# Optimization experiments

Hardware: AMD Instinct MI355X
Metric: run time of the kernel (lower is better)

## Reference

```python
import jax, jax.numpy as jnp
import numpy as np

NUM_ELEC = 128
TIME_STEPS = 128  # must equal NUM_ELEC for the original module's matmuls to be shape-consistent
NUM_VOXELS = 2052
HIDDEN = 64
DCT_DIM = 512
BATCH = 64
RHO = 0.5
TAU = 0.1
PLV_THRESH = 0.5


def dct_matrix(N, K):
    n = np.arange(N)[None, :]
    k = np.arange(K)[:, None]
    m = np.sqrt(2.0 / N) * np.cos(np.pi * (2 * n + 1) * k / (2 * N))
    m[0, :] = 1.0 / np.sqrt(N)
    return jnp.asarray(m, dtype=jnp.float32)


def setup_inputs() -> dict:
    ks = jax.random.split(jax.random.key(0), 12)
    H = HIDDEN
    return {
        "z": jax.random.normal(ks[0], (BATCH, NUM_ELEC, TIME_STEPS), dtype=jnp.float32),
        "lead_field": jax.random.normal(ks[1], (NUM_VOXELS, NUM_ELEC), dtype=jnp.float32),
        "gumbel_u": jax.random.uniform(ks[2], (NUM_ELEC, NUM_ELEC), dtype=jnp.float32, minval=1e-6, maxval=1.0 - 1e-6),
        "w_gae": jax.random.normal(ks[3], (NUM_ELEC, H), dtype=jnp.float32) / np.sqrt(NUM_ELEC),
        "b_gae": jnp.zeros((H,), dtype=jnp.float32),
        "w1": jax.random.normal(ks[4], (NUM_ELEC, H), dtype=jnp.float32) / np.sqrt(NUM_ELEC),
        "b1": jnp.zeros((H,), dtype=jnp.float32),
        "w2": jax.random.normal(ks[5], (H, H), dtype=jnp.float32) / np.sqrt(H),
        "b2": jnp.zeros((H,), dtype=jnp.float32),
        "w_ih": jax.random.normal(ks[6], (3 * H, H), dtype=jnp.float32) / np.sqrt(H),
        "w_hh": jax.random.normal(ks[7], (3 * H, H), dtype=jnp.float32) / np.sqrt(H),
        "b_ih": jnp.zeros((3 * H,), dtype=jnp.float32),
        "b_hh": jnp.zeros((3 * H,), dtype=jnp.float32),
    }


def _hilbert_phases(z):
    # FFT-based analytic signal along last axis (== scipy.signal.hilbert), then instantaneous phase
    T = z.shape[-1]
    idx = jnp.arange(T)
    hf = jnp.where(idx == 0, 1.0, jnp.where(idx < T // 2, 2.0, jnp.where(idx == T // 2, 1.0, 0.0)))
    analytic = jnp.fft.ifft(jnp.fft.fft(z, axis=-1) * hf, axis=-1)
    return jnp.angle(analytic)


def _forward(z, lead_field, gumbel_u, w_gae, b_gae, w1, b1, w2, b2, w_ih, w_hh, b_ih, b_hh):
    B, N, T = z.shape
    # ---- PLV adjacency: fused broadcast+reduction replacing the 128x128 python double loop ----
    phases = _hilbert_phases(z)                                  # [B,N,T]
    E = jnp.exp(1j * phases).astype(jnp.complex64)
    # plv[i,j] = |mean_{b,t} exp(i(phi_i - phi_j))| = |E_i . conj(E_j)| / (B*T)
    plv = jnp.abs(jnp.einsum('bit,bjt->ij', E, jnp.conj(E))) / (B * T)
    a = (plv >= PLV_THRESH).astype(jnp.float32)                  # [N,N]
    # ---- GAE: GCN encoder on batch-averaged signals + inner-product decoder ----
    x = jnp.mean(z, axis=0)                                      # [N,T] (T == N)
    hg = jax.nn.relu((a @ x) @ w_gae + b_gae)                    # [N,H]
    p = jax.nn.sigmoid(hg @ hg.T)                                # [N,N]
    # ---- Gumbel graph augmentation ----
    e = RHO * p + (1.0 - RHO) * a
    g = -jnp.log(-jnp.log(gumbel_u))
    a_aug = jax.nn.sigmoid((jnp.log(e) - jnp.log(1.0 - e) + g) / TAU)
    # ---- symmetric degree normalization ----
    d_inv_sqrt = jnp.sum(a_aug, axis=-1) ** -0.5
    a_norm = d_inv_sqrt[:, None] * a_aug * d_inv_sqrt[None, :]
    zT = jnp.swapaxes(z, 1, 2)                                   # [B,T,N]
    h = jax.nn.relu(jnp.matmul(a_norm, zT) @ w1 + b1)            # [B,N,H]
    h = jax.nn.relu(jnp.matmul(a_norm, h) @ w2 + b2)             # [B,N,H]
    h_seq = h.reshape(B * T, -1)                                 # [B*T,H]
    # ---- GRU over flattened (B*T) sequence (torch nn.GRU gate order r,z,n) ----
    Hd = w_hh.shape[1]
    def gru_step(hprev, xt):
        gi = xt @ w_ih.T + b_ih
        gh = hprev @ w_hh.T + b_hh
        ir, iz, inn = jnp.split(gi, 3)
        hr, hz, hn = jnp.split(gh, 3)
        r = jax.nn.sigmoid(ir + hr)
        zg = jax.nn.sigmoid(iz + hz)
        cand = jnp.tanh(inn + r * hn)
        hnew = (1.0 - zg) * cand + zg * hprev
        return hnew, hnew
    _, h_gru = jax.lax.scan(gru_step, jnp.zeros((Hd,), z.dtype), h_seq)
    del h_gru  # computed as in the original forward, but not part of the returned tuple
    # ---- lead-field projection + DCT low-pass reconstruction ----
    dct_m = dct_matrix(NUM_VOXELS, DCT_DIM)                      # [K,V]
    s = jnp.matmul(lead_field, zT)                               # [B,V,T]
    s_dct = jnp.matmul(dct_m, s)                                 # [B,K,T]
    s_low = s_dct[:, :DCT_DIM, :]                                # [B,K,T] (full, K == dct_dim)
    s_recon = jnp.matmul(dct_m.T, s_low)                         # [B,V,T]
    return s_low, s_recon, a_aug


def reference(z, lead_field, gumbel_u, w_gae, b_gae, w1, b1, w2, b2, w_ih, w_hh, b_ih, b_hh):
    return _forward(z, lead_field, gumbel_u, w_gae, b_gae, w1, b1, w2, b2, w_ih, w_hh, b_ih, b_hh)
```

## Files before the change

kernel.cpp:

```cpp
#include <hip/hip_runtime.h>

#define NV 2052
#define KD 512
#define RTOT 2564
#define KTOT 256
#define JTOT 8192

typedef __attribute__((ext_vector_type(8))) short short8v;
typedef __attribute__((ext_vector_type(4))) float f32x4;
typedef unsigned short ushort_t;

#define OFF_AF   0u
#define OFF_ABF  65536u
#define OFF_BBF  409600u
#define OFF_YBF  1458176u
#define OFF_PG   2506752u
#define OFF_PM1  6701056u
#define OFF_A    7749632u
#define OFF_X    7766016u
#define OFF_HG   7782400u

#define SREC_OFF 4194304u
#define AAUG_OFF 21004288u

#define GLOAD16(g, l) __builtin_amdgcn_global_load_lds( \
    (const __attribute__((address_space(1))) unsigned int*)(g), \
    (__attribute__((address_space(3))) unsigned int*)(l), 16, 0, 0)

__device__ __forceinline__ float dct_val(int k, int v) {
    if (k == 0) return 1.0f / sqrtf(2052.0f);
    int m = (2 * v + 1) * k;
    int r = m % 8208;
    float ang = (float)((double)r * (3.14159265358979323846 / 4104.0));
    return sqrtf(2.0f / 2052.0f) * cosf(ang);
}

__device__ __forceinline__ void bf16split(float x, ushort_t& hi, ushort_t& lo) {
    unsigned xb = __float_as_uint(x);
    hi = (ushort_t)(xb >> 16);
    float r = x - __uint_as_float((unsigned)hi << 16);
    lo = (ushort_t)(__float_as_uint(r) >> 16);
}

__device__ __forceinline__ ushort_t bf16rn(float x) {
    unsigned xb = __float_as_uint(x);
    return (ushort_t)((xb + 0x7fffu + ((xb >> 16) & 1u)) >> 16);
}

__global__ __launch_bounds__(256) void k_front(const float* __restrict__ LF, const float* __restrict__ z,
                                               float* __restrict__ Pm1,
                                               ushort_t* __restrict__ Ybf, ushort_t* __restrict__ Bbf) {
    __shared__ float sh[8][132];
    const int tid = threadIdx.x;
    const int bid = blockIdx.x;
    if (bid < 1024) {
        const int t = tid & 127;
        const int kk = tid >> 7;
        const int k0 = (bid & 63) * 8;
        const int vch = bid >> 6;
        const int v0 = vch * 128;
        const int nv = (vch == 15) ? 132 : 128;
        for (int p = tid; p < 1056; p += 256) {
            int rr = p / 132, cc = p - rr * 132;
            sh[rr][cc] = dct_val(k0 + rr, v0 + cc);
        }
        __syncthreads();
        const float* lf = LF + (size_t)v0 * 128 + t;
        float a0 = 0.f, a1 = 0.f, a2 = 0.f, a3 = 0.f;
        for (int vi = 0; vi + 2 <= nv; vi += 2) {
            float l0 = lf[vi * 128], l1 = lf[vi * 128 + 128];
            a0 += sh[kk + 0][vi] * l0; a1 += sh[kk + 2][vi] * l0;
            a2 += sh[kk + 4][vi] * l0; a3 += sh[kk + 6][vi] * l0;
            a0 += sh[kk + 0][vi + 1] * l1; a1 += sh[kk + 2][vi + 1] * l1;
            a2 += sh[kk + 4][vi + 1] * l1; a3 += sh[kk + 6][vi + 1] * l1;
        }
        float* P = Pm1 + (size_t)vch * 65536;
        P[(k0 + kk + 0) * 128 + t] = a0;
        P[(k0 + kk + 2) * 128 + t] = a1;
        P[(k0 + kk + 4) * 128 + t] = a2;
        P[(k0 + kk + 6) * 128 + t] = a3;
    } else {
        const int t = tid & 127;
        const int rr = tid >> 7;
        const int rid = (bid - 1024) * 2 + rr;
        const int b = rid >> 7, i = rid & 127;
        sh[rr][t] = z[(size_t)rid * 128 + t];
        if (tid < 128) {
            float hv = 0.f;
            if (t & 1) {
                float ang = 3.14159265358979323846f * (float)t * (1.0f / 128.0f);
                hv = (cosf(ang) / sinf(ang)) * (1.0f / 64.0f);
            }
            sh[2][t] = hv;
        }
        __syncthreads();
        float acc = 0.f;
        #pragma unroll 8
        for (int q = 0; q < 64; ++q) {
            int d = 2 * q + 1;
            acc += sh[2][d] * sh[rr][(t - d) & 127];
        }
        float zv = sh[rr][t];
        float inv = rsqrtf(zv * zv + acc * acc);
        Ybf[(size_t)i * JTOT + b * 128 + t] = bf16rn(zv * inv);
        Ybf[(size_t)(128 + i) * JTOT + b * 128 + t] = bf16rn(acc * inv);
        ushort_t hi = (ushort_t)(__float_as_uint(zv) >> 16);
        ushort_t* row = Bbf + (size_t)rid * KTOT;
        row[t] = hi; row[128 + t] = hi;
    }
}

__global__ __launch_bounds__(256) void k_m1red(const float* __restrict__ Pm1, float* __restrict__ AF,
                                               ushort_t* __restrict__ Abf) {
    int id = blockIdx.x * 256 + threadIdx.x;
    float s = 0.f;
    #pragma unroll
    for (int p = 0; p < 16; ++p) s += Pm1[p * 65536 + id];
    AF[id] = s;
    int rid = id >> 7, t = id & 127;
    ushort_t hi, lo; bf16split(s, hi, lo);
    ushort_t* row = Abf + (size_t)rid * KTOT;
    row[t] = hi; row[128 + t] = lo;
}

__global__ __launch_bounds__(256) void k_m2(const float* __restrict__ M1, ushort_t* __restrict__ Abf) {
    __shared__ float sd[2][128];
    const int tid = threadIdx.x;
    const int t = tid & 127;
    const int vv = tid >> 7;
    const int myv = blockIdx.x * 2 + vv;
    float a0 = 0.f, a1 = 0.f, a2 = 0.f, a3 = 0.f;
    for (int kc = 0; kc < KD; kc += 128) {
        __syncthreads();
        sd[vv][t] = dct_val(kc + t, myv);
        __syncthreads();
        const float* m1 = M1 + (size_t)kc * 128 + t;
        #pragma unroll 8
        for (int ki = 0; ki < 32; ++ki) {
            a0 += sd[vv][ki +  0] * m1[(ki +  0) * 128];
            a1 += sd[vv][ki + 32] * m1[(ki + 32) * 128];
            a2 += sd[vv][ki + 64] * m1[(ki + 64) * 128];
            a3 += sd[vv][ki + 96] * m1[(ki + 96) * 128];
        }
    }
    float s = (a0 + a1) + (a2 + a3);
    ushort_t hi, lo; bf16split(s, hi, lo);
    ushort_t* row = Abf + (size_t)(KD + myv) * KTOT;
    row[t] = hi; row[128 + t] = lo;
}

__global__ __launch_bounds__(256) void k_back(const ushort_t* __restrict__ Abf, const ushort_t* __restrict__ Bbf,
                                              const ushort_t* __restrict__ Ybf,
                                              float* __restrict__ out, float* __restrict__ Pg) {
    __shared__ float SMf[8704];
    ushort_t* Al = (ushort_t*)SMf;
    ushort_t* Bl = Al + 8192;
    const int tid = threadIdx.x;
    const int wave = tid >> 6;
    const int lane = tid & 63;
    const int wr = wave >> 1, wc = wave & 1;
    const int l15 = lane & 15;
    const int lhi = lane >> 4;
    const int bid = blockIdx.x;

    f32x4 acc[4][4];
    #pragma unroll
    for (int i = 0; i < 4; ++i)
        #pragma unroll
        for (int j = 0; j < 4; ++j)
            acc[i][j] = (f32x4){0.f, 0.f, 0.f, 0.f};

    if (bid < 1344) {
        const int j0 = (bid & 63) * 128;
        const int r0 = (bid >> 6) * 128;
        for (int kc = 0; kc < KTOT; kc += 64) {
            __syncthreads();
            #pragma unroll
            for (int i = 0; i < 4; ++i) {
                int elt = (wave * 4 + i) * 64 + lane;
                int m = elt >> 3;
                int sc = (elt & 7) ^ (m & 7);
                GLOAD16(Abf + (size_t)(r0 + m) * KTOT + kc + sc * 8, &Al[(wave * 4 + i) * 512]);
                GLOAD16(Bbf + (size_t)(j0 + m) * KTOT + kc + sc * 8, &Bl[(wave * 4 + i) * 512]);
            }
            asm volatile("s_waitcnt vmcnt(0)" ::: "memory");
            __syncthreads();
            #pragma unroll
            for (int kk = 0; kk < 2; ++kk) {
                short8v av[4], bv[4];
                #pragma unroll
                for (int mi = 0; mi < 4; ++mi) {
                    int m = wr * 64 + mi * 16 + l15;
                    int ch = (kk * 4 + lhi) ^ (m & 7);
                    av[mi] = *(const short8v*)&Al[m * 64 + ch * 8];
                }
                #pragma unroll
                for (int ni = 0; ni < 4; ++ni) {
                    int n = wc * 64 + ni * 16 + l15;
                    int ch = (kk * 4 + lhi) ^ (n & 7);
                    bv[ni] = *(const short8v*)&Bl[n * 64 + ch * 8];
                }
                #pragma unroll
                for (int mi = 0; mi < 4; ++mi)
                    #pragma unroll
                    for (int ni = 0; ni < 4; ++ni)
                        acc[mi][ni] = __builtin_amdgcn_mfma_f32_16x16x32_bf16(av[mi], bv[ni], acc[mi][ni], 0, 0, 0);
            }
        }
        const unsigned bb = (unsigned)(bid & 63);
        #pragma unroll
        for (int hhalf = 0; hhalf < 2; ++hhalf) {
            __syncthreads();
            if (wc == hhalf) {
                #pragma unroll
                for (int mi = 0; mi < 4; ++mi)
                    #pragma unroll
                    for (int ni = 0; ni < 4; ++ni)
                        #pragma unroll
                        for (int reg = 0; reg < 4; ++reg) {
                            int rl = wr * 64 + mi * 16 + lhi * 4 + reg;
                            int cl = ni * 16 + l15;
                            SMf[rl * 68 + cl] = acc[mi][ni][reg];
                        }
            }
            __syncthreads();
            int rl = tid >> 1;
            int cs = (tid & 1) * 32;
            int r = r0 + rl;
            if (r < RTOT) {
                unsigned base;
                if (r < KD) base = bb * 65536u + (unsigned)r * 128u;
                else        base = SREC_OFF + bb * 262656u + (unsigned)(r - KD) * 128u;
                base += hhalf * 64 + cs;
                const float* src = &SMf[rl * 68 + cs];
                float* dst = out + base;
                #pragma unroll
                for (int q = 0; q < 8; ++q)
                    *(float4*)(dst + q * 4) = *(const float4*)(src + q * 4);
            }
        }
    } else {
        const int g = bid - 1344;
        const int j0 = (g & 1) * 128;
        const int i0 = ((g >> 1) & 1) * 128;
        const int sk = g >> 2;
        const int kc0 = sk * 128;
        for (int kc = kc0; kc < kc0 + 128; kc += 64) {
            __syncthreads();
            #pragma unroll
            for (int i = 0; i < 4; ++i) {
                int elt = (wave * 4 + i) * 64 + lane;
                int m = elt >> 3;
                int sc = (elt & 7) ^ (m & 7);
                GLOAD16(Ybf + (size_t)(i0 + m) * JTOT + kc + sc * 8, &Al[(wave * 4 + i) * 512]);
                GLOAD16(Ybf + (size_t)(j0 + m) * JTOT + kc + sc * 8, &Bl[(wave * 4 + i) * 512]);
            }
            asm volatile("s_waitcnt vmcnt(0)" ::: "memory");
            __syncthreads();
            #pragma unroll
            for (int kk = 0; kk < 2; ++kk) {
                short8v av[4], bv[4];
                #pragma unroll
                for (int mi = 0; mi < 4; ++mi) {
                    int m = wr * 64 + mi * 16 + l15;
                    int ch = (kk * 4 + lhi) ^ (m & 7);
                    av[mi] = *(const short8v*)&Al[m * 64 + ch * 8];
                }
                #pragma unroll
                for (int ni = 0; ni < 4; ++ni) {
                    int n = wc * 64 + ni * 16 + l15;
                    int ch = (kk * 4 + lhi) ^ (n & 7);
                    bv[ni] = *(const short8v*)&Bl[n * 64 + ch * 8];
                }
                #pragma unroll
                for (int mi = 0; mi < 4; ++mi)
                    #pragma unroll
                    for (int ni = 0; ni < 4; ++ni)
                        acc[mi][ni] = __builtin_amdgcn_mfma_f32_16x16x32_bf16(av[mi], bv[ni], acc[mi][ni], 0, 0, 0);
            }
        }
        const int q = ((g >> 1) & 1) * 2 + (g & 1);
        float* P = Pg + (size_t)(sk * 4 + q) * 16384;
        #pragma unroll
        for (int mi = 0; mi < 4; ++mi)
            #pragma unroll
            for (int reg = 0; reg < 4; ++reg) {
                int rl = wr * 64 + mi * 16 + lhi * 4 + reg;
                #pragma unroll
                for (int ni = 0; ni < 4; ++ni) {
                    int cl = wc * 64 + ni * 16 + l15;
                    P[rl * 128 + cl] = acc[mi][ni][reg];
                }
            }
    }
}

__global__ __launch_bounds__(256) void k_plvx(const float* __restrict__ Pg, const float* __restrict__ z,
                                              float* __restrict__ A, float* __restrict__ X) {
    int id = blockIdx.x * 256 + threadIdx.x;
    float R = 0.f, I = 0.f;
    #pragma unroll 8
    for (int sk = 0; sk < 64; ++sk) {
        const float* P = Pg + (size_t)sk * 65536 + id;
        R += P[0] + P[3 * 16384];
        I += P[2 * 16384] - P[1 * 16384];
    }
    float plv = sqrtf(R * R + I * I) * (1.0f / 8192.0f);
    A[id] = (plv >= 0.5f) ? 1.0f : 0.0f;
    float s = 0.f;
    for (int b = 0; b < 64; ++b) s += z[(size_t)b * 16384 + id];
    X[id] = s * (1.0f / 64.0f);
}

__global__ __launch_bounds__(256) void k_axhg(const float* __restrict__ A, const float* __restrict__ X,
                                              const float* __restrict__ Wg, const float* __restrict__ bg,
                                              float* __restrict__ HG) {
    __shared__ float sAX[2][128];
    const int tid = threadIdx.x;
    const int t = tid & 127;
    const int ii = tid >> 7;
    const int i = blockIdx.x * 2 + ii;
    float s = 0.f;
    const float* arow = A + (size_t)i * 128;
    #pragma unroll 4
    for (int j = 0; j < 128; ++j) s += arow[j] * X[j * 128 + t];
    sAX[ii][t] = s;
    __syncthreads();
    if (tid < 128) {
        int i2 = tid >> 6;
        int h = tid & 63;
        float v = bg[h];
        #pragma unroll 4
        for (int t2 = 0; t2 < 128; ++t2) v += sAX[i2][t2] * Wg[t2 * 64 + h];
        HG[(size_t)(blockIdx.x * 2 + i2) * 64 + h] = fmaxf(v, 0.f);
    }
}

__global__ __launch_bounds__(256) void k_aaug(const float* __restrict__ HG, const float* __restrict__ A,
                                              const float* __restrict__ U, float* __restrict__ out) {
    int id = blockIdx.x * 256 + threadIdx.x;
    int i = id >> 7, j = id & 127;
    float dot = 0.f;
    #pragma unroll 8
    for (int h = 0; h < 64; ++h) dot += HG[i * 64 + h] * HG[j * 64 + h];
    float p = 1.f / (1.f + expf(-dot));
    float e = 0.5f * p + 0.5f * A[id];
    float gmb = -logf(-logf(U[id]));
    float arg = (logf(e) - logf(1.f - e) + gmb) * 10.0f;
    out[AAUG_OFF + id] = 1.f / (1.f + expf(-arg));
}

extern "C" void kernel_launch(void* const* d_in, const int* in_sizes, int n_in,
                              void* d_out, int out_size, void* d_ws, size_t ws_size,
                              hipStream_t stream) {
    const float* z  = (const float*)d_in[0];
    const float* LF = (const float*)d_in[1];
    const float* U  = (const float*)d_in[2];
    const float* Wg = (const float*)d_in[3];
    const float* bg = (const float*)d_in[4];
    float* out = (float*)d_out;
    float* W = (float*)d_ws;

    float* AF  = W + OFF_AF;
    ushort_t* Abf = (ushort_t*)(W + OFF_ABF);
    ushort_t* Bbf = (ushort_t*)(W + OFF_BBF);
    ushort_t* Ybf = (ushort_t*)(W + OFF_YBF);
    float* Pg  = W + OFF_PG;
    float* Pm1 = W + OFF_PM1;
    float* A   = W + OFF_A;
    float* X   = W + OFF_X;
    float* HG  = W + OFF_HG;

    k_front<<<5120, 256, 0, stream>>>(LF, z, Pm1, Ybf, Bbf);
    k_m1red<<<256, 256, 0, stream>>>(Pm1, AF, Abf);
    k_m2   <<<1026, 256, 0, stream>>>(AF, Abf);
    k_back <<<1600, 256, 0, stream>>>(Abf, Bbf, Ybf, out, Pg);
    k_plvx <<<64, 256, 0, stream>>>(Pg, z, A, X);
    k_axhg <<<64, 256, 0, stream>>>(A, X, Wg, bg, HG);
    k_aaug <<<64, 256, 0, stream>>>(HG, A, U, out);
}
```

Measured before the change: 119.3 us.

## Retune m2 register blocking, swizzle back tile order, cut PLV split-K partials

```diff
diff --git a/kernel.cpp b/kernel.cpp
--- a/kernel.cpp
+++ b/kernel.cpp
@@ -124,29 +124,41 @@
 }
 
 __global__ __launch_bounds__(256) void k_m2(const float* __restrict__ M1, ushort_t* __restrict__ Abf) {
-    __shared__ float sd[2][128];
+    __shared__ float sd[4][128];
     const int tid = threadIdx.x;
     const int t = tid & 127;
     const int vv = tid >> 7;
-    const int myv = blockIdx.x * 2 + vv;
-    float a0 = 0.f, a1 = 0.f, a2 = 0.f, a3 = 0.f;
+    const int v0 = blockIdx.x * 4;
+    float a0 = 0.f, a1 = 0.f, b0 = 0.f, b1 = 0.f;
     for (int kc = 0; kc < KD; kc += 128) {
         __syncthreads();
-        sd[vv][t] = dct_val(kc + t, myv);
+        for (int p = tid; p < 512; p += 256) {
+            int rr = p >> 7, cc = p & 127;
+            sd[rr][cc] = dct_val(kc + cc, v0 + rr);
+        }
         __syncthreads();
         const float* m1 = M1 + (size_t)kc * 128 + t;
-        #pragma unroll 8
-        for (int ki = 0; ki < 32; ++ki) {
-            a0 += sd[vv][ki +  0] * m1[(ki +  0) * 128];
-            a1 += sd[vv][ki + 32] * m1[(ki + 32) * 128];
-            a2 += sd[vv][ki + 64] * m1[(ki + 64) * 128];
-            a3 += sd[vv][ki + 96] * m1[(ki + 96) * 128];
-        }
-    }
-    float s = (a0 + a1) + (a2 + a3);
-    ushort_t hi, lo; bf16split(s, hi, lo);
-    ushort_t* row = Abf + (size_t)(KD + myv) * KTOT;
-    row[t] = hi; row[128 + t] = lo;
+        #pragma unroll 4
+        for (int ki = 0; ki < 64; ++ki) {
+            float m0 = m1[ki * 128];
+            float mv = m1[(ki + 64) * 128];
+            a0 += sd[vv][ki] * m0;      a1 += sd[vv][ki + 64] * mv;
+            b0 += sd[vv + 2][ki] * m0;  b1 += sd[vv + 2][ki + 64] * mv;
+        }
+    }
+    {
+        float s = a0 + a1; ushort_t hi, lo; bf16split(s, hi, lo);
+        ushort_t* row = Abf + (size_t)(KD + v0 + vv) * KTOT;
+        row[t] = hi; row[128 + t] = lo;
+    }
+    {
+        int myv = v0 + vv + 2;
+        float s = b0 + b1; ushort_t hi, lo; bf16split(s, hi, lo);
+        if (myv < NV) {
+            ushort_t* row = Abf + (size_t)(KD + myv) * KTOT;
+            row[t] = hi; row[128 + t] = lo;
+        }
+    }
 }
 
 __global__ __launch_bounds__(256) void k_back(const ushort_t* __restrict__ Abf, const ushort_t* __restrict__ Bbf,
@@ -171,7 +183,8 @@
             acc[i][j] = (f32x4){0.f, 0.f, 0.f, 0.f};
 
     if (bid < 1344) {
-        const int j0 = (bid & 63) * 128;
+        const int jt = ((bid & 7) << 3) + ((bid >> 3) & 7);
+        const int j0 = jt * 128;
         const int r0 = (bid >> 6) * 128;
         for (int kc = 0; kc < KTOT; kc += 64) {
             __syncthreads();
@@ -207,7 +220,7 @@
                         acc[mi][ni] = __builtin_amdgcn_mfma_f32_16x16x32_bf16(av[mi], bv[ni], acc[mi][ni], 0, 0, 0);
             }
         }
-        const unsigned bb = (unsigned)(bid & 63);
+        const unsigned bb = (unsigned)jt;
         #pragma unroll
         for (int hhalf = 0; hhalf < 2; ++hhalf) {
             __syncthreads();
@@ -244,8 +257,8 @@
         const int j0 = (g & 1) * 128;
         const int i0 = ((g >> 1) & 1) * 128;
         const int sk = g >> 2;
-        const int kc0 = sk * 128;
-        for (int kc = kc0; kc < kc0 + 128; kc += 64) {
+        const int kc0 = sk * 512;
+        for (int kc = kc0; kc < kc0 + 512; kc += 64) {
             __syncthreads();
             #pragma unroll
             for (int i = 0; i < 4; ++i) {
@@ -299,40 +312,42 @@
                                               float* __restrict__ A, float* __restrict__ X) {
     int id = blockIdx.x * 256 + threadIdx.x;
     float R = 0.f, I = 0.f;
-    #pragma unroll 8
-    for (int sk = 0; sk < 64; ++sk) {
+    #pragma unroll
+    for (int sk = 0; sk < 16; ++sk) {
         const float* P = Pg + (size_t)sk * 65536 + id;
         R += P[0] + P[3 * 16384];
         I += P[2 * 16384] - P[1 * 16384];
     }
     float plv = sqrtf(R * R + I * I) * (1.0f / 8192.0f);
     A[id] = (plv >= 0.5f) ? 1.0f : 0.0f;
-    float s = 0.f;
-    for (int b = 0; b < 64; ++b) s += z[(size_t)b * 16384 + id];
-    X[id] = s * (1.0f / 64.0f);
-}
-
-__global__ __launch_bounds__(256) void k_axhg(const float* __restrict__ A, const float* __restrict__ X,
+    float s0 = 0.f, s1 = 0.f, s2 = 0.f, s3 = 0.f;
+    #pragma unroll 4
+    for (int b = 0; b < 64; b += 4) {
+        s0 += z[(size_t)(b + 0) * 16384 + id];
+        s1 += z[(size_t)(b + 1) * 16384 + id];
+        s2 += z[(size_t)(b + 2) * 16384 + id];
+        s3 += z[(size_t)(b + 3) * 16384 + id];
+    }
+    X[id] = ((s0 + s1) + (s2 + s3)) * (1.0f / 64.0f);
+}
+
+__global__ __launch_bounds__(128) void k_axhg(const float* __restrict__ A, const float* __restrict__ X,
                                               const float* __restrict__ Wg, const float* __restrict__ bg,
                                               float* __restrict__ HG) {
-    __shared__ float sAX[2][128];
-    const int tid = threadIdx.x;
-    const int t = tid & 127;
-    const int ii = tid >> 7;
-    const int i = blockIdx.x * 2 + ii;
+    __shared__ float sAX[128];
+    const int t = threadIdx.x;
+    const int i = blockIdx.x;
+    const float* arow = A + (size_t)i * 128;
     float s = 0.f;
-    const float* arow = A + (size_t)i * 128;
     #pragma unroll 4
     for (int j = 0; j < 128; ++j) s += arow[j] * X[j * 128 + t];
-    sAX[ii][t] = s;
+    sAX[t] = s;
     __syncthreads();
-    if (tid < 128) {
-        int i2 = tid >> 6;
-        int h = tid & 63;
-        float v = bg[h];
+    if (t < 64) {
+        float v = bg[t];
         #pragma unroll 4
-        for (int t2 = 0; t2 < 128; ++t2) v += sAX[i2][t2] * Wg[t2 * 64 + h];
-        HG[(size_t)(blockIdx.x * 2 + i2) * 64 + h] = fmaxf(v, 0.f);
+        for (int t2 = 0; t2 < 128; ++t2) v += sAX[t2] * Wg[t2 * 64 + t];
+        HG[(size_t)i * 64 + t] = fmaxf(v, 0.f);
     }
 }
 
@@ -373,9 +388,9 @@
 
     k_front<<<5120, 256, 0, stream>>>(LF, z, Pm1, Ybf, Bbf);
     k_m1red<<<256, 256, 0, stream>>>(Pm1, AF, Abf);
-    k_m2   <<<1026, 256, 0, stream>>>(AF, Abf);
-    k_back <<<1600, 256, 0, stream>>>(Abf, Bbf, Ybf, out, Pg);
+    k_m2   <<<513, 256, 0, stream>>>(AF, Abf);
+    k_back <<<1408, 256, 0, stream>>>(Abf, Bbf, Ybf, out, Pg);
     k_plvx <<<64, 256, 0, stream>>>(Pg, z, A, X);
-    k_axhg <<<64, 256, 0, stream>>>(A, X, Wg, bg, HG);
+    k_axhg <<<128, 128, 0, stream>>>(A, X, Wg, bg, HG);
     k_aaug <<<64, 256, 0, stream>>>(HG, A, U, out);
 }
```

After: 125.5 us. +5.2%, slower.
